# Optimization experiments

Hardware: AMD Instinct MI355X
Metric: run time of the kernel (lower is better)

## Reference

```python
import jax, jax.numpy as jnp
import numpy as np

B = 32768      # number of graphs in the batch
NPG = 54       # nodes per graph (fixed by reshape(batch_size, 54*4))
EPG = 144      # directed edges per graph (Catan board: 72 undirected)
N = B * NPG
E = B * EPG
GLOB = 10


def _lin(k, fan_in, fan_out):
    lim = 1.0 / np.sqrt(fan_in)
    kw, kb = jax.random.split(k)
    W = jax.random.uniform(kw, (fan_in, fan_out), jnp.float32, -lim, lim)
    b = jax.random.uniform(kb, (fan_out,), jnp.float32, -lim, lim)
    return W, b


def setup_inputs() -> dict:
    key = jax.random.key(0)
    ks = jax.random.split(key, 16)
    x = jax.random.normal(ks[0], (N, 8), jnp.float32)
    # PyG-style batched edge_index: edges stay within each 54-node block
    base = (jnp.arange(B, dtype=jnp.int32) * NPG)[:, None]
    src = (jax.random.randint(ks[1], (B, EPG), 0, NPG, jnp.int32) + base).reshape(-1)
    dst = (jax.random.randint(ks[2], (B, EPG), 0, NPG, jnp.int32) + base).reshape(-1)
    edge_index = jnp.stack([src, dst], axis=0)
    edge_attr = jax.random.uniform(ks[3], (E,), jnp.float32)
    globalFeats = jax.random.normal(ks[4], (B, GLOB), jnp.float32)
    # GraphConv 1: in=8 -> hidden=16  (lin_rel has bias, lin_root has no bias)
    W_rel1, b1 = _lin(ks[5], 8, 16)
    W_root1, _ = _lin(ks[6], 8, 16)
    # GraphConv 2: 16 -> 4
    W_rel2, b2 = _lin(ks[7], 16, 4)
    W_root2, _ = _lin(ks[8], 16, 4)
    # Global MLP: 10 -> 8 -> 8 -> 10
    Wg1, bg1 = _lin(ks[9], GLOB, 8)
    Wg2, bg2 = _lin(ks[10], 8, 8)
    Wg3, bg3 = _lin(ks[11], 8, GLOB)
    # Out MLP: 54*4 + 10 = 226 -> 128 -> 1
    Wo1, bo1 = _lin(ks[12], NPG * 4 + GLOB, 128)
    Wo2, bo2 = _lin(ks[13], 128, 1)
    return dict(x=x, edge_index=edge_index, edge_attr=edge_attr,
                globalFeats=globalFeats,
                W_rel1=W_rel1, b1=b1, W_root1=W_root1,
                W_rel2=W_rel2, b2=b2, W_root2=W_root2,
                Wg1=Wg1, bg1=bg1, Wg2=Wg2, bg2=bg2, Wg3=Wg3, bg3=bg3,
                Wo1=Wo1, bo1=bo1, Wo2=Wo2, bo2=bo2, isTrain=0)


def _graph_conv(x, src, dst, edge_attr, W_rel, b, W_root):
    # PyG GraphConv (aggr='add'): out = lin_rel(sum_j w_ij * x_j) + lin_root(x)
    msg = edge_attr[:, None] * x[src]                       # [E, F_in]
    agg = jax.ops.segment_sum(msg, dst, num_segments=N)     # [N, F_in]
    return agg @ W_rel + b + x @ W_root


def reference(x, edge_index, edge_attr, globalFeats,
              W_rel1, b1, W_root1, W_rel2, b2, W_root2,
              Wg1, bg1, Wg2, bg2, Wg3, bg3, Wo1, bo1, Wo2, bo2, isTrain):
    src, dst = edge_index[0], edge_index[1]
    h = jax.nn.relu(_graph_conv(x, src, dst, edge_attr, W_rel1, b1, W_root1))
    h = jax.nn.relu(_graph_conv(h, src, dst, edge_attr, W_rel2, b2, W_root2))
    embeds = h.reshape(B, NPG * 4)                          # [B, 216]
    g = jax.nn.relu(globalFeats @ Wg1 + bg1)
    g = jax.nn.relu(g @ Wg2 + bg2)
    g = jax.nn.relu(g @ Wg3 + bg3)
    out = jnp.concatenate([embeds, g], axis=-1)             # [B, 226]
    # dropout p=0.2 with isTrain=0 (eval) -> identity
    out = jax.nn.relu(out @ Wo1 + bo1)
    out = jax.nn.sigmoid(out @ Wo2 + bo2)                   # [B, 1]
    return out
```

## Files before the change

### kernel.cpp

```cpp
#include <hip/hip_runtime.h>
#include <hip/hip_fp16.h>
#include <math.h>

#define NPG 54
#define EPG 144
#define GLOB 10
#define VROW 216
#define GPB 2

typedef _Float16 f16x8 __attribute__((ext_vector_type(8)));
typedef _Float16 f16x4 __attribute__((ext_vector_type(4)));
typedef float    f32x4 __attribute__((ext_vector_type(4)));

#define WSYNC() asm volatile("s_waitcnt lgkmcnt(0)" ::: "memory")

struct __align__(16) GL {
    _Float16 Adj[NPG][56];
    _Float16 XH[16][72];
};

__global__ __launch_bounds__(128, 5) void graph_kernel(
    const float* __restrict__ x,
    const int*   __restrict__ edge_index,
    const float* __restrict__ edge_attr,
    const float* __restrict__ W_rel1, const float* __restrict__ b1,
    const float* __restrict__ W_root1,
    const float* __restrict__ W_rel2, const float* __restrict__ b2,
    const float* __restrict__ W_root2,
    _Float16* __restrict__ v_out,
    int E_total)
{
    __shared__ GL S[GPB];
    const int tid  = threadIdx.x;
    const int w    = tid >> 6;
    const int lane = tid & 63;
    const int ln15 = lane & 15;
    const int quad = lane >> 4;
    const int g    = blockIdx.x * GPB + w;
    GL& L = S[w];
    const int nbase = g * NPG;
    const int ebase = g * EPG;

    _Float16 (*cat)[40] = (_Float16(*)[40])&L.Adj[0][0];

    int   esrc_r[3], edst_r[3];
    float ea_r[3];
    #pragma unroll
    for (int k = 0; k < 3; k++) {
        int e = lane + 64 * k;
        if (e < EPG) {
            esrc_r[k] = edge_index[ebase + e] - nbase;
            edst_r[k] = edge_index[(size_t)E_total + ebase + e] - nbase;
            ea_r[k]   = edge_attr[ebase + e];
        } else { esrc_r[k] = 0; edst_r[k] = -1; ea_r[k] = 0.0f; }
    }
    f16x8 xv = {0, 0, 0, 0, 0, 0, 0, 0};
    if (lane < NPG) {
        const float4* xg4 = (const float4*)(x + (size_t)(nbase + lane) * 8);
        float4 lo = xg4[0], hi = xg4[1];
        xv = (f16x8){ (_Float16)lo.x, (_Float16)lo.y, (_Float16)lo.z, (_Float16)lo.w,
                      (_Float16)hi.x, (_Float16)hi.y, (_Float16)hi.z, (_Float16)hi.w };
    }

    f16x8 wf1 = {0, 0, 0, 0, 0, 0, 0, 0};
    if (quad == 0) {
        #pragma unroll
        for (int j = 0; j < 8; j++) wf1[j] = (_Float16)W_rel1[j * 16 + ln15];
    } else if (quad == 1) {
        #pragma unroll
        for (int j = 0; j < 8; j++) wf1[j] = (_Float16)W_root1[j * 16 + ln15];
    }
    f16x8 wf2 = {0, 0, 0, 0, 0, 0, 0, 0};
    if (ln15 < 4) {
        #pragma unroll
        for (int j = 0; j < 8; j++) {
            int k = quad * 8 + j;
            wf2[j] = (_Float16)((k < 16) ? W_rel2[k * 4 + ln15]
                                         : W_root2[(k - 16) * 4 + ln15]);
        }
    }
    const float b1v = b1[ln15];
    const float b2v = b2[ln15 & 3];

    {
        uint4* z = (uint4*)&L;
        #pragma unroll
        for (int i = lane; i < 522; i += 64) z[i] = make_uint4(0, 0, 0, 0);
    }
    if (lane < NPG) {
        #pragma unroll
        for (int f = 0; f < 8; f++) L.XH[f][lane] = xv[f];
    }
    WSYNC();

    #pragma unroll
    for (int k = 0; k < 3; k++) {
        if (edst_r[k] >= 0) {
            int s = esrc_r[k];
            __half2* cell = (__half2*)&L.Adj[edst_r[k]][s & ~1];
            __half a16 = __float2half(ea_r[k]);
            __half z16 = __float2half(0.0f);
            __half2 val = (s & 1) ? __halves2half2(z16, a16)
                                  : __halves2half2(a16, z16);
            unsafeAtomicAdd(cell, val);
        }
    }
    WSYNC();

    f16x8 af[4][2];
    #pragma unroll
    for (int t = 0; t < 4; t++)
        #pragma unroll
        for (int ks = 0; ks < 2; ks++)
            af[t][ks] = *(const f16x8*)&L.Adj[t * 16 + ln15][ks * 32 + quad * 8];
    WSYNC();

    if (lane < NPG) *(f16x8*)&cat[lane][8] = xv;

    f32x4 acc1[4];
    #pragma unroll
    for (int t = 0; t < 4; t++) acc1[t] = (f32x4){0.f, 0.f, 0.f, 0.f};
    #pragma unroll
    for (int ks = 0; ks < 2; ks++) {
        f16x8 bx = *(const f16x8*)&L.XH[ln15][ks * 32 + quad * 8];
        #pragma unroll
        for (int t = 0; t < 4; t++)
            acc1[t] = __builtin_amdgcn_mfma_f32_16x16x32_f16(af[t][ks], bx, acc1[t], 0, 0, 0);
    }
    #pragma unroll
    for (int t = 0; t < 4; t++)
        #pragma unroll
        for (int r = 0; r < 4; r++)
            if (ln15 < 8) cat[t * 16 + quad * 4 + r][ln15] = (_Float16)acc1[t][r];
    WSYNC();

    f32x4 accL[4];
    #pragma unroll
    for (int t = 0; t < 4; t++) {
        f16x8 al = *(const f16x8*)&cat[t * 16 + ln15][quad * 8];
        f32x4 ci = (f32x4){b1v, b1v, b1v, b1v};
        accL[t] = __builtin_amdgcn_mfma_f32_16x16x32_f16(al, wf1, ci, 0, 0, 0);
    }
    #pragma unroll
    for (int t = 0; t < 4; t++) {
        f16x4 hp;
        #pragma unroll
        for (int r = 0; r < 4; r++) {
            int node = t * 16 + quad * 4 + r;
            float h = (node < NPG) ? fmaxf(accL[t][r], 0.0f) : 0.0f;
            hp[r] = (_Float16)h;
            cat[node][16 + ln15] = (_Float16)h;
        }
        *(f16x4*)&L.XH[ln15][t * 16 + quad * 4] = hp;
    }
    WSYNC();

    f32x4 acc2[4];
    #pragma unroll
    for (int t = 0; t < 4; t++) acc2[t] = (f32x4){0.f, 0.f, 0.f, 0.f};
    #pragma unroll
    for (int ks = 0; ks < 2; ks++) {
        f16x8 bh = *(const f16x8*)&L.XH[ln15][ks * 32 + quad * 8];
        #pragma unroll
        for (int t = 0; t < 4; t++)
            acc2[t] = __builtin_amdgcn_mfma_f32_16x16x32_f16(af[t][ks], bh, acc2[t], 0, 0, 0);
    }
    #pragma unroll
    for (int t = 0; t < 4; t++)
        #pragma unroll
        for (int r = 0; r < 4; r++)
            cat[t * 16 + quad * 4 + r][ln15] = (_Float16)acc2[t][r];
    WSYNC();

    _Float16* vt = &L.XH[0][0];
    #pragma unroll
    for (int t = 0; t < 4; t++) {
        f16x8 a2 = *(const f16x8*)&cat[t * 16 + ln15][quad * 8];
        f32x4 ci = (f32x4){b2v, b2v, b2v, b2v};
        f32x4 h2 = __builtin_amdgcn_mfma_f32_16x16x32_f16(a2, wf2, ci, 0, 0, 0);
        #pragma unroll
        for (int r = 0; r < 4; r++) {
            int node = t * 16 + quad * 4 + r;
            if (ln15 < 4 && node < NPG)
                vt[node * 4 + ln15] = (_Float16)fmaxf(h2[r], 0.0f);
        }
    }
    WSYNC();

    if (lane < 27)
        *(f16x8*)(v_out + (size_t)g * VROW + lane * 8) = *(const f16x8*)&vt[lane * 8];
}

#define BTS 264

__global__ __launch_bounds__(512) void out_mlp_mfma(
    const _Float16* __restrict__ V,
    const float* __restrict__ gf,
    const float* __restrict__ Wg1, const float* __restrict__ bg1,
    const float* __restrict__ Wg2, const float* __restrict__ bg2,
    const float* __restrict__ Wg3, const float* __restrict__ bg3,
    const float* __restrict__ Wo1,
    const float* __restrict__ bo1,
    const float* __restrict__ Wo2,
    const float* __restrict__ bo2,
    float* __restrict__ out)
{
    extern __shared__ _Float16 Bt[];

    const int tid  = threadIdx.x;
    const int w    = tid >> 6;
    const int lane = tid & 63;
    const int ln15 = lane & 15;
    const int quad = lane >> 4;
    const int row0 = blockIdx.x * 128;
    const int row  = row0 + w * 16 + ln15;

    float bo1v[8], wo2v[8];
    #pragma unroll
    for (int t = 0; t < 8; t++) {
        bo1v[t] = bo1[t * 16 + ln15];
        wo2v[t] = Wo2[t * 16 + ln15];
    }
    const float bo2v = bo2[0];

    float t3[GLOB];
    {
        const float* gr = gf + (size_t)row * GLOB;
        float t0[GLOB];
        #pragma unroll
        for (int i = 0; i < GLOB; i++) t0[i] = gr[i];
        float t1[8];
        #pragma unroll
        for (int j = 0; j < 8; j++) {
            float a = bg1[j];
            #pragma unroll
            for (int i = 0; i < GLOB; i++) a += t0[i] * Wg1[i * 8 + j];
            t1[j] = fmaxf(a, 0.0f);
        }
        float t2[8];
        #pragma unroll
        for (int j = 0; j < 8; j++) {
            float a = bg2[j];
            #pragma unroll
            for (int i = 0; i < 8; i++) a += t1[i] * Wg2[i * 8 + j];
            t2[j] = fmaxf(a, 0.0f);
        }
        #pragma unroll
        for (int j = 0; j < GLOB; j++) {
            float a = bg3[j];
            #pragma unroll
            for (int i = 0; i < 8; i++) a += t2[i] * Wg3[i * GLOB + j];
            t3[j] = fmaxf(a, 0.0f);
        }
    }

    const _Float16* Arow = V + (size_t)row * VROW;
    f16x8 af[8];
    #pragma unroll
    for (int s = 0; s < 6; s++)
        af[s] = *(const f16x8*)(Arow + s * 32 + quad * 8);
    if (quad == 3)
        af[6] = (f16x8){ (_Float16)t3[0], (_Float16)t3[1], (_Float16)t3[2], (_Float16)t3[3],
                         (_Float16)t3[4], (_Float16)t3[5], (_Float16)t3[6], (_Float16)t3[7] };
    else
        af[6] = *(const f16x8*)(Arow + 192 + quad * 8);
    af[7] = (f16x8){0, 0, 0, 0, 0, 0, 0, 0};
    if (quad == 0) { af[7][0] = (_Float16)t3[8]; af[7][1] = (_Float16)t3[9]; }

    {
        int4* bz = (int4*)Bt;
        for (int i = tid; i < 4224; i += 512)
            bz[i] = make_int4(0, 0, 0, 0);
    }
    __syncthreads();
    for (int i = tid; i < 7232; i += 512) {
        int k  = i >> 5;
        int nq = (i & 31) * 4;
        float4 v = *(const float4*)(Wo1 + (size_t)k * 128 + nq);
        Bt[(nq + 0) * BTS + k] = (_Float16)v.x;
        Bt[(nq + 1) * BTS + k] = (_Float16)v.y;
        Bt[(nq + 2) * BTS + k] = (_Float16)v.z;
        Bt[(nq + 3) * BTS + k] = (_Float16)v.w;
    }
    __syncthreads();

    f32x4 acc[8];
    #pragma unroll
    for (int t = 0; t < 8; t++) acc[t] = (f32x4){0.f, 0.f, 0.f, 0.f};

    for (int s = 0; s < 8; s++) {
        #pragma unroll
        for (int t = 0; t < 8; t++) {
            f16x8 bf = *(const f16x8*)&Bt[(t * 16 + ln15) * BTS + s * 32 + quad * 8];
            acc[t] = __builtin_amdgcn_mfma_f32_16x16x32_f16(af[s], bf, acc[t], 0, 0, 0);
        }
    }

    #pragma unroll
    for (int rr = 0; rr < 4; rr++) {
        float p = 0.0f;
        #pragma unroll
        for (int t = 0; t < 8; t++) {
            float h = fmaxf(acc[t][rr] + bo1v[t], 0.0f);
            p += h * wo2v[t];
        }
        p += __shfl_xor(p, 1);
        p += __shfl_xor(p, 2);
        p += __shfl_xor(p, 4);
        p += __shfl_xor(p, 8);
        if (ln15 == rr) {
            int orow = row0 + w * 16 + quad * 4 + rr;
            out[orow] = 1.0f / (1.0f + expf(-(p + bo2v)));
        }
    }
}

extern "C" void kernel_launch(void* const* d_in, const int* in_sizes, int n_in,
                              void* d_out, int out_size, void* d_ws, size_t ws_size,
                              hipStream_t stream) {
    const float* x        = (const float*)d_in[0];
    const int*   ei       = (const int*)  d_in[1];
    const float* ea       = (const float*)d_in[2];
    const float* gf       = (const float*)d_in[3];
    const float* W_rel1   = (const float*)d_in[4];
    const float* b1       = (const float*)d_in[5];
    const float* W_root1  = (const float*)d_in[6];
    const float* W_rel2   = (const float*)d_in[7];
    const float* b2       = (const float*)d_in[8];
    const float* W_root2  = (const float*)d_in[9];
    const float* Wg1      = (const float*)d_in[10];
    const float* bg1      = (const float*)d_in[11];
    const float* Wg2      = (const float*)d_in[12];
    const float* bg2      = (const float*)d_in[13];
    const float* Wg3      = (const float*)d_in[14];
    const float* bg3      = (const float*)d_in[15];
    const float* Wo1      = (const float*)d_in[16];
    const float* bo1      = (const float*)d_in[17];
    const float* Wo2      = (const float*)d_in[18];
    const float* bo2      = (const float*)d_in[19];

    float* out   = (float*)d_out;
    _Float16* V  = (_Float16*)d_ws;

    const int B = out_size;
    const int E = in_sizes[1] / 2;

    graph_kernel<<<B / GPB, 128, 0, stream>>>(
        x, ei, ea,
        W_rel1, b1, W_root1, W_rel2, b2, W_root2,
        V, E);

    out_mlp_mfma<<<B / 128, 512, 128 * BTS * sizeof(_Float16), stream>>>(
        V, gf, Wg1, bg1, Wg2, bg2, Wg3, bg3, Wo1, bo1, Wo2, bo2, out);
}
```

Baseline: 217.7 us.

## Transpose MFMA operand roles in graph kernel to vectorize LDS stores and outputs

Swaps the A and B operands of every MFMA so each lane owns a node column instead of a row. Accumulator results can then be written with packed f16x4 stores rather than scalar per-element stores, and the final layer writes straight to global memory, dropping the staging buffer and last sync. Layer-1 x operands are loaded directly from global into registers instead of a transposed LDS tile. The cost is more scalar global loads of x per lane and a larger padded H1T buffer to zero.

Measured after the change: 252.7 us. 16.1% more time.

```diff
diff --git a/kernel.cpp b/kernel.cpp
--- a/kernel.cpp
+++ b/kernel.cpp
@@ -16,7 +16,7 @@
 
 struct __align__(16) GL {
     _Float16 Adj[NPG][56];
-    _Float16 XH[16][72];
+    _Float16 H1T[16][88];
 };
 
 __global__ __launch_bounds__(128, 5) void graph_kernel(
@@ -41,7 +41,8 @@
     const int nbase = g * NPG;
     const int ebase = g * EPG;
 
-    _Float16 (*cat)[40] = (_Float16(*)[40])&L.Adj[0][0];
+    _Float16* adjp = &L.Adj[0][0];
+    _Float16 (*cat)[40] = (_Float16(*)[40])adjp;
 
     int   esrc_r[3], edst_r[3];
     float ea_r[3];
@@ -54,6 +55,17 @@
             ea_r[k]   = edge_attr[ebase + e];
         } else { esrc_r[k] = 0; edst_r[k] = -1; ea_r[k] = 0.0f; }
     }
+    f16x8 xA[2];
+    #pragma unroll
+    for (int c = 0; c < 2; c++) {
+        #pragma unroll
+        for (int m = 0; m < 8; m++) {
+            int src = c * 32 + quad * 8 + m;
+            float v = 0.0f;
+            if (ln15 < 8 && src < NPG) v = x[(size_t)(nbase + src) * 8 + ln15];
+            xA[c][m] = (_Float16)v;
+        }
+    }
     f16x8 xv = {0, 0, 0, 0, 0, 0, 0, 0};
     if (lane < NPG) {
         const float4* xg4 = (const float4*)(x + (size_t)(nbase + lane) * 8);
@@ -79,17 +91,12 @@
                                          : W_root2[(k - 16) * 4 + ln15]);
         }
     }
-    const float b1v = b1[ln15];
-    const float b2v = b2[ln15 & 3];
+    const float4 b1q = *(const float4*)(b1 + quad * 4);
+    const float4 b2q = *(const float4*)b2;
 
     {
         uint4* z = (uint4*)&L;
-        #pragma unroll
-        for (int i = lane; i < 522; i += 64) z[i] = make_uint4(0, 0, 0, 0);
-    }
-    if (lane < NPG) {
-        #pragma unroll
-        for (int f = 0; f < 8; f++) L.XH[f][lane] = xv[f];
+        for (int i = lane; i < 554; i += 64) z[i] = make_uint4(0, 0, 0, 0);
     }
     WSYNC();
 
@@ -111,84 +118,81 @@
     #pragma unroll
     for (int t = 0; t < 4; t++)
         #pragma unroll
-        for (int ks = 0; ks < 2; ks++)
-            af[t][ks] = *(const f16x8*)&L.Adj[t * 16 + ln15][ks * 32 + quad * 8];
-    WSYNC();
-
+        for (int c = 0; c < 2; c++)
+            af[t][c] = *(const f16x8*)(adjp + (t * 16 + ln15) * 56 + c * 32 + quad * 8);
+    WSYNC();
+
+    f32x4 acc1[4];
+    #pragma unroll
+    for (int t = 0; t < 4; t++) acc1[t] = (f32x4){0.f, 0.f, 0.f, 0.f};
+    #pragma unroll
+    for (int c = 0; c < 2; c++)
+        #pragma unroll
+        for (int t = 0; t < 4; t++)
+            acc1[t] = __builtin_amdgcn_mfma_f32_16x16x32_f16(xA[c], af[t][c], acc1[t], 0, 0, 0);
+    if (quad < 2) {
+        #pragma unroll
+        for (int t = 0; t < 4; t++) {
+            f16x4 ap;
+            #pragma unroll
+            for (int r = 0; r < 4; r++) ap[r] = (_Float16)acc1[t][r];
+            *(f16x4*)&cat[t * 16 + ln15][quad * 4] = ap;
+        }
+    }
     if (lane < NPG) *(f16x8*)&cat[lane][8] = xv;
-
-    f32x4 acc1[4];
-    #pragma unroll
-    for (int t = 0; t < 4; t++) acc1[t] = (f32x4){0.f, 0.f, 0.f, 0.f};
-    #pragma unroll
-    for (int ks = 0; ks < 2; ks++) {
-        f16x8 bx = *(const f16x8*)&L.XH[ln15][ks * 32 + quad * 8];
+    WSYNC();
+
+    f32x4 ci1 = {b1q.x, b1q.y, b1q.z, b1q.w};
+    #pragma unroll
+    for (int t = 0; t < 4; t++) {
+        f16x8 bc = *(const f16x8*)&cat[t * 16 + ln15][quad * 8];
+        f32x4 hL = __builtin_amdgcn_mfma_f32_16x16x32_f16(wf1, bc, ci1, 0, 0, 0);
+        int node = t * 16 + ln15;
+        f16x4 hp;
+        #pragma unroll
+        for (int r = 0; r < 4; r++) hp[r] = (_Float16)fmaxf(hL[r], 0.0f);
+        *(f16x4*)&cat[node][16 + quad * 4] = hp;
+        if (node < NPG) {
+            #pragma unroll
+            for (int r = 0; r < 4; r++) L.H1T[quad * 4 + r][node] = hp[r];
+        }
+    }
+    WSYNC();
+
+    f16x8 hA[2];
+    #pragma unroll
+    for (int c = 0; c < 2; c++)
+        hA[c] = *(const f16x8*)&L.H1T[ln15][c * 32 + quad * 8];
+    f32x4 acc2[4];
+    #pragma unroll
+    for (int t = 0; t < 4; t++) acc2[t] = (f32x4){0.f, 0.f, 0.f, 0.f};
+    #pragma unroll
+    for (int c = 0; c < 2; c++)
         #pragma unroll
         for (int t = 0; t < 4; t++)
-            acc1[t] = __builtin_amdgcn_mfma_f32_16x16x32_f16(af[t][ks], bx, acc1[t], 0, 0, 0);
-    }
-    #pragma unroll
-    for (int t = 0; t < 4; t++)
-        #pragma unroll
-        for (int r = 0; r < 4; r++)
-            if (ln15 < 8) cat[t * 16 + quad * 4 + r][ln15] = (_Float16)acc1[t][r];
-    WSYNC();
-
-    f32x4 accL[4];
+            acc2[t] = __builtin_amdgcn_mfma_f32_16x16x32_f16(hA[c], af[t][c], acc2[t], 0, 0, 0);
     #pragma unroll
     for (int t = 0; t < 4; t++) {
-        f16x8 al = *(const f16x8*)&cat[t * 16 + ln15][quad * 8];
-        f32x4 ci = (f32x4){b1v, b1v, b1v, b1v};
-        accL[t] = __builtin_amdgcn_mfma_f32_16x16x32_f16(al, wf1, ci, 0, 0, 0);
-    }
+        f16x4 ap;
+        #pragma unroll
+        for (int r = 0; r < 4; r++) ap[r] = (_Float16)acc2[t][r];
+        *(f16x4*)&cat[t * 16 + ln15][quad * 4] = ap;
+    }
+    WSYNC();
+
+    f32x4 ci2 = {b2q.x, b2q.y, b2q.z, b2q.w};
     #pragma unroll
     for (int t = 0; t < 4; t++) {
-        f16x4 hp;
-        #pragma unroll
-        for (int r = 0; r < 4; r++) {
-            int node = t * 16 + quad * 4 + r;
-            float h = (node < NPG) ? fmaxf(accL[t][r], 0.0f) : 0.0f;
-            hp[r] = (_Float16)h;
-            cat[node][16 + ln15] = (_Float16)h;
-        }
-        *(f16x4*)&L.XH[ln15][t * 16 + quad * 4] = hp;
-    }
-    WSYNC();
-
-    f32x4 acc2[4];
-    #pragma unroll
-    for (int t = 0; t < 4; t++) acc2[t] = (f32x4){0.f, 0.f, 0.f, 0.f};
-    #pragma unroll
-    for (int ks = 0; ks < 2; ks++) {
-        f16x8 bh = *(const f16x8*)&L.XH[ln15][ks * 32 + quad * 8];
-        #pragma unroll
-        for (int t = 0; t < 4; t++)
-            acc2[t] = __builtin_amdgcn_mfma_f32_16x16x32_f16(af[t][ks], bh, acc2[t], 0, 0, 0);
-    }
-    #pragma unroll
-    for (int t = 0; t < 4; t++)
-        #pragma unroll
-        for (int r = 0; r < 4; r++)
-            cat[t * 16 + quad * 4 + r][ln15] = (_Float16)acc2[t][r];
-    WSYNC();
-
-    _Float16* vt = &L.XH[0][0];
-    #pragma unroll
-    for (int t = 0; t < 4; t++) {
-        f16x8 a2 = *(const f16x8*)&cat[t * 16 + ln15][quad * 8];
-        f32x4 ci = (f32x4){b2v, b2v, b2v, b2v};
-        f32x4 h2 = __builtin_amdgcn_mfma_f32_16x16x32_f16(a2, wf2, ci, 0, 0, 0);
-        #pragma unroll
-        for (int r = 0; r < 4; r++) {
-            int node = t * 16 + quad * 4 + r;
-            if (ln15 < 4 && node < NPG)
-                vt[node * 4 + ln15] = (_Float16)fmaxf(h2[r], 0.0f);
-        }
-    }
-    WSYNC();
-
-    if (lane < 27)
-        *(f16x8*)(v_out + (size_t)g * VROW + lane * 8) = *(const f16x8*)&vt[lane * 8];
+        int node = t * 16 + ln15;
+        f16x8 bv = *(const f16x8*)&cat[node][quad * 8];
+        f32x4 o = __builtin_amdgcn_mfma_f32_16x16x32_f16(wf2, bv, ci2, 0, 0, 0);
+        if (quad == 0 && node < NPG) {
+            f16x4 vp;
+            #pragma unroll
+            for (int r = 0; r < 4; r++) vp[r] = (_Float16)fmaxf(o[r], 0.0f);
+            *(f16x4*)(v_out + (size_t)g * VROW + node * 4) = vp;
+        }
+    }
 }
 
 #define BTS 264
```
